# Kernel optimization log

Hardware: AMD Instinct MI355X
Metric: run time of the kernel (lower is better)

The kernel has to match this reference:

```python
import jax, jax.numpy as jnp
import numpy as np

N_NODES = 100000
D_IN = 64
D_OUT = 64
N_EDGES = 1250000


def setup_inputs() -> dict:
    key = jax.random.key(0)
    k_x, k_e, k_wl, k_bl, k_wr = jax.random.split(key, 5)
    x = jax.random.normal(k_x, (N_NODES, D_IN), dtype=jnp.float32)
    edge_index = jax.random.randint(k_e, (2, N_EDGES), 0, N_NODES, dtype=jnp.int64)
    # SAGEConv params: lin_l (neighbor transform, with bias), lin_r (root transform, no bias)
    s_in = 1.0 / np.sqrt(D_IN)
    W_l = jax.random.uniform(k_wl, (D_IN, D_OUT), dtype=jnp.float32, minval=-s_in, maxval=s_in)
    b_l = jax.random.uniform(k_bl, (D_OUT,), dtype=jnp.float32, minval=-s_in, maxval=s_in)
    W_r = jax.random.uniform(k_wr, (D_IN, D_OUT), dtype=jnp.float32, minval=-s_in, maxval=s_in)
    return {"x": x, "edge_index": edge_index, "W_l": W_l, "b_l": b_l, "W_r": W_r}


def reference(x, edge_index, W_l, b_l, W_r):
    # PyG SAGEConv with aggr='add':
    #   out = lin_l(sum_{j in N(i)} x_j) + lin_r(x_i), then tanh
    src = edge_index[0]  # message sources (x_j)
    dst = edge_index[1]  # message targets (i)
    msg = x[src]                                             # [E, D_IN] gather
    aggr = jax.ops.segment_sum(msg, dst, num_segments=x.shape[0])  # [N, D_IN] scatter-add
    out = aggr @ W_l + b_l + x @ W_r                         # [N, D_OUT]
    return jnp.tanh(out)
```

## Files before the change

kernel.cpp:

```cpp
#include <hip/hip_runtime.h>
#include <hip/hip_bf16.h>
#include <hip/hip_fp16.h>

#define N_NODES 100000
#define D 64
#define N_EDGES 1250000

#define RB 64
#define NB 1563
#define FCAP 1536
#define SORT_CAP 1536

#define CB_SHIFT 11
#define NCB 49
#define CCAP 28672
#define FINE_PER_COARSE 32

#define CPAD 16

#define EPB 4096
#define PARTA_BLOCKS ((N_EDGES + EPB - 1) / EPB)
#define SEGS 16
#define SEG_CAP 1792

#define TN 64
#define PRE_BLOCKS 1563
#define FUSED_BLOCKS (PARTA_BLOCKS + PRE_BLOCKS)

#define XP 72

#define SMEM_BYTES 27648

typedef unsigned short ushort_t;
typedef _Float16 half_t;
typedef __attribute__((ext_vector_type(8))) _Float16 half8;
typedef __attribute__((ext_vector_type(4))) float floatx4;

__global__ __launch_bounds__(256) void pre_part_kernel(
    const float* __restrict__ x, const float* __restrict__ W_l,
    const float* __restrict__ b_l, const float* __restrict__ W_r,
    ushort_t* __restrict__ y, ushort_t* __restrict__ z,
    const int* __restrict__ src, const int* __restrict__ dst,
    int* __restrict__ ccursor, unsigned* __restrict__ coarse,
    int N, int E)
{
    extern __shared__ char smem[];
    int t = threadIdx.x;

    if (blockIdx.x < PARTA_BLOCKS) {
        int* hist4        = (int*)smem;
        int* lbase        = (int*)(smem + 1024);
        int* gbase        = (int*)(smem + 1280);
        int* lwb          = (int*)(smem + 1536);
        unsigned* sortedL = (unsigned*)(smem + 2560);
        const int w = t >> 6;

        if (t < 4 * NCB) hist4[t] = 0;
        __syncthreads();

        int base = blockIdx.x * EPB;
        int lim = E - base; if (lim > EPB) lim = EPB;

        for (int i = t; i < lim; i += 256)
            atomicAdd(&hist4[w * NCB + (dst[base + i] >> CB_SHIFT)], 1);
        __syncthreads();

        if (t < 64) {
            int c0 = 0, c1 = 0, c2 = 0, c3 = 0, tot = 0;
            if (t < NCB) {
                c0 = hist4[t]; c1 = hist4[NCB + t];
                c2 = hist4[2 * NCB + t]; c3 = hist4[3 * NCB + t];
                tot = c0 + c1 + c2 + c3;
            }
            int inc = tot;
#pragma unroll
            for (int off = 1; off < 64; off <<= 1) {
                int n = __shfl_up(inc, off, 64);
                if (t >= off) inc += n;
            }
            int ex = inc - tot;
            if (t < NCB) {
                lbase[t] = ex;
                gbase[t] = tot ? atomicAdd(&ccursor[t * CPAD], tot) : 0;
                lwb[t]           = ex;
                lwb[NCB + t]     = ex + c0;
                lwb[2 * NCB + t] = ex + c0 + c1;
                lwb[3 * NCB + t] = ex + c0 + c1 + c2;
            } else {
                lbase[t] = lim;
            }
        }
        __syncthreads();

        for (int i = t; i < lim; i += 256) {
            int d = dst[base + i];
            int s = src[base + i];
            int b = d >> CB_SHIFT;
            int pos = atomicSub(&hist4[w * NCB + b], 1) - 1;
            sortedL[lwb[w * NCB + b] + pos] =
                (unsigned)s | ((unsigned)(d & ((1 << CB_SHIFT) - 1)) << 17);
        }
        __syncthreads();

        for (int i = t; i < lim; i += 256) {
            int lo = 0;
#pragma unroll
            for (int s2 = 32; s2; s2 >>= 1) {
                int c = lo + s2;
                if (c < 64 && lbase[c] <= i) lo = c;
            }
            coarse[(size_t)lo * CCAP + gbase[lo] + (i - lbase[lo])] = sortedL[i];
        }
        return;
    }

    half_t* sWt = (half_t*)smem;
    half_t* sXh = (half_t*)(smem + 18432);

    for (int i = t; i < 64 * 64; i += 256) {
        int k = i >> 6, c = i & 63;
        sWt[c * XP + k]        = (half_t)W_l[i];
        sWt[(64 + c) * XP + k] = (half_t)W_r[i];
    }

    long base = (long)(blockIdx.x - PARTA_BLOCKS) * TN;
    for (int i = t; i < TN * 16; i += 256) {
        int n = i >> 4, q = i & 15;
        long node = base + n;
        float4 v = make_float4(0.f, 0.f, 0.f, 0.f);
        if (node < N) v = ((const float4*)(x + node * D))[q];
        half_t* p = &sXh[n * XP + q * 4];
        p[0] = (half_t)v.x; p[1] = (half_t)v.y;
        p[2] = (half_t)v.z; p[3] = (half_t)v.w;
    }
    __syncthreads();

    const int lane  = t & 63;
    const int w     = t >> 6;
    const int col16 = lane & 15;
    const int quad  = lane >> 4;

    const int nrow = w * 16 + col16;
    half8 xb0 = *(half8*)&sXh[nrow * XP + quad * 8];
    half8 xb1 = *(half8*)&sXh[nrow * XP + 32 + quad * 8];

    float4 bq[4];
#pragma unroll
    for (int j = 0; j < 4; j++) bq[j] = *(const float4*)(b_l + j * 16 + quad * 4);

#pragma unroll
    for (int ct = 0; ct < 4; ct++) {
        int c = ct * 16 + col16;
        half8 wa0 = *(half8*)&sWt[c * XP + quad * 8];
        half8 wa1 = *(half8*)&sWt[c * XP + 32 + quad * 8];
        floatx4 acc = {0.f, 0.f, 0.f, 0.f};
        acc = __builtin_amdgcn_mfma_f32_16x16x32_f16(wa0, xb0, acc, 0, 0, 0);
        acc = __builtin_amdgcn_mfma_f32_16x16x32_f16(wa1, xb1, acc, 0, 0, 0);
        union { half_t h[4]; uint2 u; } pk;
        pk.h[0] = (half_t)acc[0]; pk.h[1] = (half_t)acc[1];
        pk.h[2] = (half_t)acc[2]; pk.h[3] = (half_t)acc[3];
        *(uint2*)&sXh[(w * 16 + col16) * XP + ct * 16 + quad * 4] = pk.u;
    }
    __syncthreads();

    for (int c2 = t; c2 < TN * 8; c2 += 256) {
        int row = c2 >> 3, f = c2 & 7;
        if (base + row < N)
            *(uint4*)(y + (base + row) * D + f * 8) = *(uint4*)&sXh[row * XP + f * 8];
    }
    __syncthreads();

#pragma unroll
    for (int ct = 4; ct < 8; ct++) {
        int c = ct * 16 + col16;
        half8 wa0 = *(half8*)&sWt[c * XP + quad * 8];
        half8 wa1 = *(half8*)&sWt[c * XP + 32 + quad * 8];
        floatx4 acc = {0.f, 0.f, 0.f, 0.f};
        acc = __builtin_amdgcn_mfma_f32_16x16x32_f16(wa0, xb0, acc, 0, 0, 0);
        acc = __builtin_amdgcn_mfma_f32_16x16x32_f16(wa1, xb1, acc, 0, 0, 0);
        float4 bv = bq[ct - 4];
        union { half_t h[4]; uint2 u; } pk;
        pk.h[0] = (half_t)(acc[0] + bv.x); pk.h[1] = (half_t)(acc[1] + bv.y);
        pk.h[2] = (half_t)(acc[2] + bv.z); pk.h[3] = (half_t)(acc[3] + bv.w);
        *(uint2*)&sXh[(w * 16 + col16) * XP + (ct - 4) * 16 + quad * 4] = pk.u;
    }
    __syncthreads();

    for (int c2 = t; c2 < TN * 8; c2 += 256) {
        int row = c2 >> 3, f = c2 & 7;
        if (base + row < N)
            *(uint4*)(z + (base + row) * D + f * 8) = *(uint4*)&sXh[row * XP + f * 8];
    }
}

__global__ __launch_bounds__(256) void partB_kernel(
    const unsigned* __restrict__ coarse, const int* __restrict__ ccursor,
    int* __restrict__ fcursor, unsigned* __restrict__ fine)
{
    __shared__ int hist4[4 * FINE_PER_COARSE];
    __shared__ int lbase2[FINE_PER_COARSE];
    __shared__ int gbase2[FINE_PER_COARSE];
    __shared__ int lwb2[4 * FINE_PER_COARSE];
    __shared__ unsigned sortedL[SEG_CAP];

    int cb = blockIdx.x >> 4;
    int seg = blockIdx.x & 15;
    int t = threadIdx.x;
    const int w = t >> 6;

    int cnt = ccursor[cb * CPAD];
    int segLen = (cnt + SEGS - 1) / SEGS;
    int beg = seg * segLen;
    int end = beg + segLen; if (end > cnt) end = cnt;
    int lim = end - beg; if (lim < 0) lim = 0;

    if (t < 4 * FINE_PER_COARSE) hist4[t] = 0;
    __syncthreads();

    const unsigned* __restrict__ slab = coarse + (size_t)cb * CCAP + beg;

    for (int i = t; i < lim; i += 256)
        atomicAdd(&hist4[w * FINE_PER_COARSE + ((slab[i] >> 17) >> 6)], 1);
    __syncthreads();

    if (t < 64) {
        int c0 = 0, c1 = 0, c2 = 0, c3 = 0, tot = 0;
        if (t < FINE_PER_COARSE) {
            c0 = hist4[t]; c1 = hist4[FINE_PER_COARSE + t];
            c2 = hist4[2 * FINE_PER_COARSE + t]; c3 = hist4[3 * FINE_PER_COARSE + t];
            tot = c0 + c1 + c2 + c3;
        }
        int inc = tot;
#pragma unroll
        for (int off = 1; off < 32; off <<= 1) {
            int n = __shfl_up(inc, off, 64);
            if (t >= off) inc += n;
        }
        int ex = inc - tot;
        if (t < FINE_PER_COARSE) {
            lbase2[t] = ex;
            int fb = cb * FINE_PER_COARSE + t;
            gbase2[t] = tot ? atomicAdd(&fcursor[fb * CPAD], tot) : 0;
            lwb2[t]                       = ex;
            lwb2[FINE_PER_COARSE + t]     = ex + c0;
            lwb2[2 * FINE_PER_COARSE + t] = ex + c0 + c1;
            lwb2[3 * FINE_PER_COARSE + t] = ex + c0 + c1 + c2;
        }
    }
    __syncthreads();

    for (int i = t; i < lim; i += 256) {
        unsigned e = slab[i];
        unsigned cl = e >> 17;
        int loc = cl >> 6;
        int pos = atomicSub(&hist4[w * FINE_PER_COARSE + loc], 1) - 1;
        sortedL[lwb2[w * FINE_PER_COARSE + loc] + pos] =
            (e & 0x1FFFFu) | ((cl & 63u) << 17);
    }
    __syncthreads();

    for (int i = t; i < lim; i += 256) {
        int lo = 0;
#pragma unroll
        for (int s2 = 16; s2; s2 >>= 1) {
            int c = lo + s2;
            if (c < FINE_PER_COARSE && lbase2[c] <= i) lo = c;
        }
        fine[((size_t)cb * FINE_PER_COARSE + lo) * FCAP + gbase2[lo] + (i - lbase2[lo])]
            = sortedL[i];
    }
}

__global__ __launch_bounds__(512) void sortgather_kernel(
    const ushort_t* __restrict__ y, const ushort_t* __restrict__ z,
    const unsigned* __restrict__ part, const int* __restrict__ cursor,
    float* __restrict__ out, int N)
{
    __shared__ int sorted[SORT_CAP];
    __shared__ int hist[RB];
    __shared__ int cur[RB];
    __shared__ int begL[RB];

    int b = blockIdx.x;
    int t = threadIdx.x;
    int cnt = cursor[b * CPAD];
    if (cnt > SORT_CAP) cnt = SORT_CAP;
    const unsigned* __restrict__ slab = part + (size_t)b * FCAP;

    unsigned e0 = 0, e1 = 0, e2 = 0;
    int i0 = t, i1 = t + 512, i2 = t + 1024;
    if (i0 < cnt) e0 = slab[i0];
    if (i1 < cnt) e1 = slab[i1];
    if (i2 < cnt) e2 = slab[i2];

    if (t < RB) hist[t] = 0;
    __syncthreads();

    if (i0 < cnt) atomicAdd(&hist[e0 >> 17], 1);
    if (i1 < cnt) atomicAdd(&hist[e1 >> 17], 1);
    if (i2 < cnt) atomicAdd(&hist[e2 >> 17], 1);
    __syncthreads();

    if (t < RB) {
        int v = hist[t];
        int inc = v;
#pragma unroll
        for (int off = 1; off < RB; off <<= 1) {
            int n = __shfl_up(inc, off, RB);
            if (t >= off) inc += n;
        }
        int ex = inc - v;
        cur[t] = ex;
        begL[t] = ex;
    }
    __syncthreads();

    if (i0 < cnt) { int p = atomicAdd(&cur[e0 >> 17], 1); sorted[p] = (int)(e0 & 0x1FFFF); }
    if (i1 < cnt) { int p = atomicAdd(&cur[e1 >> 17], 1); sorted[p] = (int)(e1 & 0x1FFFF); }
    if (i2 < cnt) { int p = atomicAdd(&cur[e2 >> 17], 1); sorted[p] = (int)(e2 & 0x1FFFF); }
    __syncthreads();

    const int g = t >> 3;
    const int f = t & 7;
    int myBeg = begL[g];
    int myDeg = hist[g];

    float2 acc0 = make_float2(0.f, 0.f), acc1 = acc0, acc2 = acc0, acc3 = acc0;

#define ACC(r) { \
    float2 c0 = __half22float2(*(const __half2*)&(r).x); \
    float2 c1 = __half22float2(*(const __half2*)&(r).y); \
    float2 c2 = __half22float2(*(const __half2*)&(r).z); \
    float2 c3 = __half22float2(*(const __half2*)&(r).w); \
    acc0.x += c0.x; acc0.y += c0.y; acc1.x += c1.x; acc1.y += c1.y; \
    acc2.x += c2.x; acc2.y += c2.y; acc3.x += c3.x; acc3.y += c3.y; }

    int i = 0;
    for (; i + 8 <= myDeg; i += 8) {
        int s0 = sorted[myBeg + i];
        int s1 = sorted[myBeg + i + 1];
        int s2 = sorted[myBeg + i + 2];
        int s3 = sorted[myBeg + i + 3];
        int s4 = sorted[myBeg + i + 4];
        int s5 = sorted[myBeg + i + 5];
        int s6 = sorted[myBeg + i + 6];
        int s7 = sorted[myBeg + i + 7];
        uint4 r0 = ((const uint4*)(y + (size_t)s0 * D))[f];
        uint4 r1 = ((const uint4*)(y + (size_t)s1 * D))[f];
        uint4 r2 = ((const uint4*)(y + (size_t)s2 * D))[f];
        uint4 r3 = ((const uint4*)(y + (size_t)s3 * D))[f];
        uint4 r4 = ((const uint4*)(y + (size_t)s4 * D))[f];
        uint4 r5 = ((const uint4*)(y + (size_t)s5 * D))[f];
        uint4 r6 = ((const uint4*)(y + (size_t)s6 * D))[f];
        uint4 r7 = ((const uint4*)(y + (size_t)s7 * D))[f];
        ACC(r0) ACC(r1) ACC(r2) ACC(r3) ACC(r4) ACC(r5) ACC(r6) ACC(r7)
    }
    for (; i + 4 <= myDeg; i += 4) {
        int s0 = sorted[myBeg + i];
        int s1 = sorted[myBeg + i + 1];
        int s2 = sorted[myBeg + i + 2];
        int s3 = sorted[myBeg + i + 3];
        uint4 r0 = ((const uint4*)(y + (size_t)s0 * D))[f];
        uint4 r1 = ((const uint4*)(y + (size_t)s1 * D))[f];
        uint4 r2 = ((const uint4*)(y + (size_t)s2 * D))[f];
        uint4 r3 = ((const uint4*)(y + (size_t)s3 * D))[f];
        ACC(r0) ACC(r1) ACC(r2) ACC(r3)
    }
    for (; i < myDeg; i++) {
        int s = sorted[myBeg + i];
        uint4 r = ((const uint4*)(y + (size_t)s * D))[f];
        ACC(r)
    }
#undef ACC

    long gn = (long)b * RB + g;
    if (gn < N) {
        uint4 zr = ((const uint4*)(z + (size_t)gn * D))[f];
        float2 z0 = __half22float2(*(const __half2*)&zr.x);
        float2 z1 = __half22float2(*(const __half2*)&zr.y);
        float2 z2 = __half22float2(*(const __half2*)&zr.z);
        float2 z3 = __half22float2(*(const __half2*)&zr.w);
        float4 o0, o1;
        o0.x = tanhf(acc0.x + z0.x); o0.y = tanhf(acc0.y + z0.y);
        o0.z = tanhf(acc1.x + z1.x); o0.w = tanhf(acc1.y + z1.y);
        o1.x = tanhf(acc2.x + z2.x); o1.y = tanhf(acc2.y + z2.y);
        o1.z = tanhf(acc3.x + z3.x); o1.w = tanhf(acc3.y + z3.y);
        float4* op = (float4*)(out + gn * D);
        op[2 * f] = o0;
        op[2 * f + 1] = o1;
    }
}

extern "C" void kernel_launch(void* const* d_in, const int* in_sizes, int n_in,
                              void* d_out, int out_size, void* d_ws, size_t ws_size,
                              hipStream_t stream) {
    const float* x   = (const float*)d_in[0];
    const int* ei    = (const int*)d_in[1];
    const float* W_l = (const float*)d_in[2];
    const float* b_l = (const float*)d_in[3];
    const float* W_r = (const float*)d_in[4];
    float* out = (float*)d_out;

    const int N = N_NODES;
    const int E = N_EDGES;
    const int* src = ei;
    const int* dst = ei + E;

    char* ws = (char*)d_ws;
    ushort_t* y      = (ushort_t*)(ws);
    ushort_t* z      = (ushort_t*)(ws + 12800000);
    unsigned* coarse = (unsigned*)(ws + 25600000);
    unsigned* fine   = (unsigned*)(ws + 31219712);
    int* ccursor     = (int*)(ws + 40822784);
    int* fcursor     = (int*)(ws + 40825920);

    hipMemsetAsync(ccursor, 0, 103168, stream);

    pre_part_kernel<<<FUSED_BLOCKS, 256, SMEM_BYTES, stream>>>(
        x, W_l, b_l, W_r, y, z, src, dst, ccursor, coarse, N, E);
    partB_kernel<<<NCB * SEGS, 256, 0, stream>>>(coarse, ccursor, fcursor, fine);
    sortgather_kernel<<<NB, 512, 0, stream>>>(y, z, fine, fcursor, out, N);
}
```

Baseline: 140.7 us.

## Enlarge fused pre/partition blocks to 1024 threads and batch sortgather buckets

```diff
diff --git a/kernel.cpp b/kernel.cpp
--- a/kernel.cpp
+++ b/kernel.cpp
@@ -18,25 +18,29 @@
 
 #define CPAD 16
 
-#define EPB 4096
+#define EPB 8192
 #define PARTA_BLOCKS ((N_EDGES + EPB - 1) / EPB)
 #define SEGS 16
 #define SEG_CAP 1792
 
-#define TN 64
-#define PRE_BLOCKS 1563
+#define TNP 256
+#define PRE_BLOCKS ((N_NODES + TNP - 1) / TNP)
 #define FUSED_BLOCKS (PARTA_BLOCKS + PRE_BLOCKS)
 
+#define NWAVE 16
+
 #define XP 72
-
-#define SMEM_BYTES 27648
+#define SMEM_BYTES 55296
+
+#define SG_BPB 2
+#define SG_BLOCKS ((NB + SG_BPB - 1) / SG_BPB)
 
 typedef unsigned short ushort_t;
 typedef _Float16 half_t;
 typedef __attribute__((ext_vector_type(8))) _Float16 half8;
 typedef __attribute__((ext_vector_type(4))) float floatx4;
 
-__global__ __launch_bounds__(256) void pre_part_kernel(
+__global__ __launch_bounds__(1024) void pre_part_kernel(
     const float* __restrict__ x, const float* __restrict__ W_l,
     const float* __restrict__ b_l, const float* __restrict__ W_r,
     ushort_t* __restrict__ y, ushort_t* __restrict__ z,
@@ -48,29 +52,28 @@
     int t = threadIdx.x;
 
     if (blockIdx.x < PARTA_BLOCKS) {
-        int* hist4        = (int*)smem;
-        int* lbase        = (int*)(smem + 1024);
-        int* gbase        = (int*)(smem + 1280);
-        int* lwb          = (int*)(smem + 1536);
-        unsigned* sortedL = (unsigned*)(smem + 2560);
+        int* hist16       = (int*)smem;
+        int* lbase        = (int*)(smem + 3200);
+        int* gbase        = (int*)(smem + 3456);
+        int* lwb          = (int*)(smem + 3712);
+        unsigned* sortedL = (unsigned*)(smem + 6912);
         const int w = t >> 6;
 
-        if (t < 4 * NCB) hist4[t] = 0;
+        if (t < NWAVE * NCB) hist16[t] = 0;
         __syncthreads();
 
         int base = blockIdx.x * EPB;
         int lim = E - base; if (lim > EPB) lim = EPB;
 
-        for (int i = t; i < lim; i += 256)
-            atomicAdd(&hist4[w * NCB + (dst[base + i] >> CB_SHIFT)], 1);
+        for (int i = t; i < lim; i += 1024)
+            atomicAdd(&hist16[w * NCB + (dst[base + i] >> CB_SHIFT)], 1);
         __syncthreads();
 
         if (t < 64) {
-            int c0 = 0, c1 = 0, c2 = 0, c3 = 0, tot = 0;
+            int cw[NWAVE]; int tot = 0;
             if (t < NCB) {
-                c0 = hist4[t]; c1 = hist4[NCB + t];
-                c2 = hist4[2 * NCB + t]; c3 = hist4[3 * NCB + t];
-                tot = c0 + c1 + c2 + c3;
+#pragma unroll
+                for (int k = 0; k < NWAVE; k++) { cw[k] = hist16[k * NCB + t]; tot += cw[k]; }
             }
             int inc = tot;
 #pragma unroll
@@ -82,27 +85,26 @@
             if (t < NCB) {
                 lbase[t] = ex;
                 gbase[t] = tot ? atomicAdd(&ccursor[t * CPAD], tot) : 0;
-                lwb[t]           = ex;
-                lwb[NCB + t]     = ex + c0;
-                lwb[2 * NCB + t] = ex + c0 + c1;
-                lwb[3 * NCB + t] = ex + c0 + c1 + c2;
+                int run = ex;
+#pragma unroll
+                for (int k = 0; k < NWAVE; k++) { lwb[k * NCB + t] = run; run += cw[k]; }
             } else {
                 lbase[t] = lim;
             }
         }
         __syncthreads();
 
-        for (int i = t; i < lim; i += 256) {
+        for (int i = t; i < lim; i += 1024) {
             int d = dst[base + i];
             int s = src[base + i];
             int b = d >> CB_SHIFT;
-            int pos = atomicSub(&hist4[w * NCB + b], 1) - 1;
+            int pos = atomicSub(&hist16[w * NCB + b], 1) - 1;
             sortedL[lwb[w * NCB + b] + pos] =
                 (unsigned)s | ((unsigned)(d & ((1 << CB_SHIFT) - 1)) << 17);
         }
         __syncthreads();
 
-        for (int i = t; i < lim; i += 256) {
+        for (int i = t; i < lim; i += 1024) {
             int lo = 0;
 #pragma unroll
             for (int s2 = 32; s2; s2 >>= 1) {
@@ -117,14 +119,14 @@
     half_t* sWt = (half_t*)smem;
     half_t* sXh = (half_t*)(smem + 18432);
 
-    for (int i = t; i < 64 * 64; i += 256) {
+    for (int i = t; i < 64 * 64; i += 1024) {
         int k = i >> 6, c = i & 63;
         sWt[c * XP + k]        = (half_t)W_l[i];
         sWt[(64 + c) * XP + k] = (half_t)W_r[i];
     }
 
-    long base = (long)(blockIdx.x - PARTA_BLOCKS) * TN;
-    for (int i = t; i < TN * 16; i += 256) {
+    long base = (long)(blockIdx.x - PARTA_BLOCKS) * TNP;
+    for (int i = t; i < TNP * 16; i += 1024) {
         int n = i >> 4, q = i & 15;
         long node = base + n;
         float4 v = make_float4(0.f, 0.f, 0.f, 0.f);
@@ -159,11 +161,11 @@
         union { half_t h[4]; uint2 u; } pk;
         pk.h[0] = (half_t)acc[0]; pk.h[1] = (half_t)acc[1];
         pk.h[2] = (half_t)acc[2]; pk.h[3] = (half_t)acc[3];
-        *(uint2*)&sXh[(w * 16 + col16) * XP + ct * 16 + quad * 4] = pk.u;
-    }
-    __syncthreads();
-
-    for (int c2 = t; c2 < TN * 8; c2 += 256) {
+        *(uint2*)&sXh[nrow * XP + ct * 16 + quad * 4] = pk.u;
+    }
+    __syncthreads();
+
+    for (int c2 = t; c2 < TNP * 8; c2 += 1024) {
         int row = c2 >> 3, f = c2 & 7;
         if (base + row < N)
             *(uint4*)(y + (base + row) * D + f * 8) = *(uint4*)&sXh[row * XP + f * 8];
@@ -182,11 +184,11 @@
         union { half_t h[4]; uint2 u; } pk;
         pk.h[0] = (half_t)(acc[0] + bv.x); pk.h[1] = (half_t)(acc[1] + bv.y);
         pk.h[2] = (half_t)(acc[2] + bv.z); pk.h[3] = (half_t)(acc[3] + bv.w);
-        *(uint2*)&sXh[(w * 16 + col16) * XP + (ct - 4) * 16 + quad * 4] = pk.u;
-    }
-    __syncthreads();
-
-    for (int c2 = t; c2 < TN * 8; c2 += 256) {
+        *(uint2*)&sXh[nrow * XP + (ct - 4) * 16 + quad * 4] = pk.u;
+    }
+    __syncthreads();
+
+    for (int c2 = t; c2 < TNP * 8; c2 += 1024) {
         int row = c2 >> 3, f = c2 & 7;
         if (base + row < N)
             *(uint4*)(z + (base + row) * D + f * 8) = *(uint4*)&sXh[row * XP + f * 8];
@@ -281,113 +283,119 @@
     __shared__ int cur[RB];
     __shared__ int begL[RB];
 
-    int b = blockIdx.x;
     int t = threadIdx.x;
-    int cnt = cursor[b * CPAD];
-    if (cnt > SORT_CAP) cnt = SORT_CAP;
-    const unsigned* __restrict__ slab = part + (size_t)b * FCAP;
-
-    unsigned e0 = 0, e1 = 0, e2 = 0;
-    int i0 = t, i1 = t + 512, i2 = t + 1024;
-    if (i0 < cnt) e0 = slab[i0];
-    if (i1 < cnt) e1 = slab[i1];
-    if (i2 < cnt) e2 = slab[i2];
-
-    if (t < RB) hist[t] = 0;
-    __syncthreads();
-
-    if (i0 < cnt) atomicAdd(&hist[e0 >> 17], 1);
-    if (i1 < cnt) atomicAdd(&hist[e1 >> 17], 1);
-    if (i2 < cnt) atomicAdd(&hist[e2 >> 17], 1);
-    __syncthreads();
-
-    if (t < RB) {
-        int v = hist[t];
-        int inc = v;
-#pragma unroll
-        for (int off = 1; off < RB; off <<= 1) {
-            int n = __shfl_up(inc, off, RB);
-            if (t >= off) inc += n;
-        }
-        int ex = inc - v;
-        cur[t] = ex;
-        begL[t] = ex;
-    }
-    __syncthreads();
-
-    if (i0 < cnt) { int p = atomicAdd(&cur[e0 >> 17], 1); sorted[p] = (int)(e0 & 0x1FFFF); }
-    if (i1 < cnt) { int p = atomicAdd(&cur[e1 >> 17], 1); sorted[p] = (int)(e1 & 0x1FFFF); }
-    if (i2 < cnt) { int p = atomicAdd(&cur[e2 >> 17], 1); sorted[p] = (int)(e2 & 0x1FFFF); }
-    __syncthreads();
-
-    const int g = t >> 3;
-    const int f = t & 7;
-    int myBeg = begL[g];
-    int myDeg = hist[g];
-
-    float2 acc0 = make_float2(0.f, 0.f), acc1 = acc0, acc2 = acc0, acc3 = acc0;
+
+    for (int sub = 0; sub < SG_BPB; sub++) {
+        int b = blockIdx.x * SG_BPB + sub;
+        if (b >= NB) break;
+        __syncthreads();
+
+        int cnt = cursor[b * CPAD];
+        if (cnt > SORT_CAP) cnt = SORT_CAP;
+        const unsigned* __restrict__ slab = part + (size_t)b * FCAP;
+
+        unsigned e0 = 0, e1 = 0, e2 = 0;
+        int i0 = t, i1 = t + 512, i2 = t + 1024;
+        if (i0 < cnt) e0 = slab[i0];
+        if (i1 < cnt) e1 = slab[i1];
+        if (i2 < cnt) e2 = slab[i2];
+
+        if (t < RB) hist[t] = 0;
+        __syncthreads();
+
+        if (i0 < cnt) atomicAdd(&hist[e0 >> 17], 1);
+        if (i1 < cnt) atomicAdd(&hist[e1 >> 17], 1);
+        if (i2 < cnt) atomicAdd(&hist[e2 >> 17], 1);
+        __syncthreads();
+
+        if (t < RB) {
+            int v = hist[t];
+            int inc = v;
+#pragma unroll
+            for (int off = 1; off < RB; off <<= 1) {
+                int n = __shfl_up(inc, off, RB);
+                if (t >= off) inc += n;
+            }
+            int ex = inc - v;
+            cur[t] = ex;
+            begL[t] = ex;
+        }
+        __syncthreads();
+
+        if (i0 < cnt) { int p = atomicAdd(&cur[e0 >> 17], 1); sorted[p] = (int)(e0 & 0x1FFFF); }
+        if (i1 < cnt) { int p = atomicAdd(&cur[e1 >> 17], 1); sorted[p] = (int)(e1 & 0x1FFFF); }
+        if (i2 < cnt) { int p = atomicAdd(&cur[e2 >> 17], 1); sorted[p] = (int)(e2 & 0x1FFFF); }
+        __syncthreads();
+
+        const int g = t >> 3;
+        const int f = t & 7;
+        int myBeg = begL[g];
+        int myDeg = hist[g];
+
+        float2 acc0 = make_float2(0.f, 0.f), acc1 = acc0, acc2 = acc0, acc3 = acc0;
 
 #define ACC(r) { \
-    float2 c0 = __half22float2(*(const __half2*)&(r).x); \
-    float2 c1 = __half22float2(*(const __half2*)&(r).y); \
-    float2 c2 = __half22float2(*(const __half2*)&(r).z); \
-    float2 c3 = __half22float2(*(const __half2*)&(r).w); \
-    acc0.x += c0.x; acc0.y += c0.y; acc1.x += c1.x; acc1.y += c1.y; \
-    acc2.x += c2.x; acc2.y += c2.y; acc3.x += c3.x; acc3.y += c3.y; }
-
-    int i = 0;
-    for (; i + 8 <= myDeg; i += 8) {
-        int s0 = sorted[myBeg + i];
-        int s1 = sorted[myBeg + i + 1];
-        int s2 = sorted[myBeg + i + 2];
-        int s3 = sorted[myBeg + i + 3];
-        int s4 = sorted[myBeg + i + 4];
-        int s5 = sorted[myBeg + i + 5];
-        int s6 = sorted[myBeg + i + 6];
-        int s7 = sorted[myBeg + i + 7];
-        uint4 r0 = ((const uint4*)(y + (size_t)s0 * D))[f];
-        uint4 r1 = ((const uint4*)(y + (size_t)s1 * D))[f];
-        uint4 r2 = ((const uint4*)(y + (size_t)s2 * D))[f];
-        uint4 r3 = ((const uint4*)(y + (size_t)s3 * D))[f];
-        uint4 r4 = ((const uint4*)(y + (size_t)s4 * D))[f];
-        uint4 r5 = ((const uint4*)(y + (size_t)s5 * D))[f];
-        uint4 r6 = ((const uint4*)(y + (size_t)s6 * D))[f];
-        uint4 r7 = ((const uint4*)(y + (size_t)s7 * D))[f];
-        ACC(r0) ACC(r1) ACC(r2) ACC(r3) ACC(r4) ACC(r5) ACC(r6) ACC(r7)
-    }
-    for (; i + 4 <= myDeg; i += 4) {
-        int s0 = sorted[myBeg + i];
-        int s1 = sorted[myBeg + i + 1];
-        int s2 = sorted[myBeg + i + 2];
-        int s3 = sorted[myBeg + i + 3];
-        uint4 r0 = ((const uint4*)(y + (size_t)s0 * D))[f];
-        uint4 r1 = ((const uint4*)(y + (size_t)s1 * D))[f];
-        uint4 r2 = ((const uint4*)(y + (size_t)s2 * D))[f];
-        uint4 r3 = ((const uint4*)(y + (size_t)s3 * D))[f];
-        ACC(r0) ACC(r1) ACC(r2) ACC(r3)
-    }
-    for (; i < myDeg; i++) {
-        int s = sorted[myBeg + i];
-        uint4 r = ((const uint4*)(y + (size_t)s * D))[f];
-        ACC(r)
-    }
+        float2 c0 = __half22float2(*(const __half2*)&(r).x); \
+        float2 c1 = __half22float2(*(const __half2*)&(r).y); \
+        float2 c2 = __half22float2(*(const __half2*)&(r).z); \
+        float2 c3 = __half22float2(*(const __half2*)&(r).w); \
+        acc0.x += c0.x; acc0.y += c0.y; acc1.x += c1.x; acc1.y += c1.y; \
+        acc2.x += c2.x; acc2.y += c2.y; acc3.x += c3.x; acc3.y += c3.y; }
+
+        int i = 0;
+        for (; i + 8 <= myDeg; i += 8) {
+            int s0 = sorted[myBeg + i];
+            int s1 = sorted[myBeg + i + 1];
+            int s2 = sorted[myBeg + i + 2];
+            int s3 = sorted[myBeg + i + 3];
+            int s4 = sorted[myBeg + i + 4];
+            int s5 = sorted[myBeg + i + 5];
+            int s6 = sorted[myBeg + i + 6];
+            int s7 = sorted[myBeg + i + 7];
+            uint4 r0 = ((const uint4*)(y + (size_t)s0 * D))[f];
+            uint4 r1 = ((const uint4*)(y + (size_t)s1 * D))[f];
+            uint4 r2 = ((const uint4*)(y + (size_t)s2 * D))[f];
+            uint4 r3 = ((const uint4*)(y + (size_t)s3 * D))[f];
+            uint4 r4 = ((const uint4*)(y + (size_t)s4 * D))[f];
+            uint4 r5 = ((const uint4*)(y + (size_t)s5 * D))[f];
+            uint4 r6 = ((const uint4*)(y + (size_t)s6 * D))[f];
+            uint4 r7 = ((const uint4*)(y + (size_t)s7 * D))[f];
+            ACC(r0) ACC(r1) ACC(r2) ACC(r3) ACC(r4) ACC(r5) ACC(r6) ACC(r7)
+        }
+        for (; i + 4 <= myDeg; i += 4) {
+            int s0 = sorted[myBeg + i];
+            int s1 = sorted[myBeg + i + 1];
+            int s2 = sorted[myBeg + i + 2];
+            int s3 = sorted[myBeg + i + 3];
+            uint4 r0 = ((const uint4*)(y + (size_t)s0 * D))[f];
+            uint4 r1 = ((const uint4*)(y + (size_t)s1 * D))[f];
+            uint4 r2 = ((const uint4*)(y + (size_t)s2 * D))[f];
+            uint4 r3 = ((const uint4*)(y + (size_t)s3 * D))[f];
+            ACC(r0) ACC(r1) ACC(r2) ACC(r3)
+        }
+        for (; i < myDeg; i++) {
+            int s = sorted[myBeg + i];
+            uint4 r = ((const uint4*)(y + (size_t)s * D))[f];
+            ACC(r)
+        }
 #undef ACC
 
-    long gn = (long)b * RB + g;
-    if (gn < N) {
-        uint4 zr = ((const uint4*)(z + (size_t)gn * D))[f];
-        float2 z0 = __half22float2(*(const __half2*)&zr.x);
-        float2 z1 = __half22float2(*(const __half2*)&zr.y);
-        float2 z2 = __half22float2(*(const __half2*)&zr.z);
-        float2 z3 = __half22float2(*(const __half2*)&zr.w);
-        float4 o0, o1;
-        o0.x = tanhf(acc0.x + z0.x); o0.y = tanhf(acc0.y + z0.y);
-        o0.z = tanhf(acc1.x + z1.x); o0.w = tanhf(acc1.y + z1.y);
-        o1.x = tanhf(acc2.x + z2.x); o1.y = tanhf(acc2.y + z2.y);
-        o1.z = tanhf(acc3.x + z3.x); o1.w = tanhf(acc3.y + z3.y);
-        float4* op = (float4*)(out + gn * D);
-        op[2 * f] = o0;
-        op[2 * f + 1] = o1;
+        long gn = (long)b * RB + g;
+        if (gn < N) {
+            uint4 zr = ((const uint4*)(z + (size_t)gn * D))[f];
+            float2 z0 = __half22float2(*(const __half2*)&zr.x);
+            float2 z1 = __half22float2(*(const __half2*)&zr.y);
+            float2 z2 = __half22float2(*(const __half2*)&zr.z);
+            float2 z3 = __half22float2(*(const __half2*)&zr.w);
+            float4 o0, o1;
+            o0.x = tanhf(acc0.x + z0.x); o0.y = tanhf(acc0.y + z0.y);
+            o0.z = tanhf(acc1.x + z1.x); o0.w = tanhf(acc1.y + z1.y);
+            o1.x = tanhf(acc2.x + z2.x); o1.y = tanhf(acc2.y + z2.y);
+            o1.z = tanhf(acc3.x + z3.x); o1.w = tanhf(acc3.y + z3.y);
+            float4* op = (float4*)(out + gn * D);
+            op[2 * f] = o0;
+            op[2 * f + 1] = o1;
+        }
     }
 }
 
@@ -416,8 +424,8 @@
 
     hipMemsetAsync(ccursor, 0, 103168, stream);
 
-    pre_part_kernel<<<FUSED_BLOCKS, 256, SMEM_BYTES, stream>>>(
+    pre_part_kernel<<<FUSED_BLOCKS, 1024, SMEM_BYTES, stream>>>(
         x, W_l, b_l, W_r, y, z, src, dst, ccursor, coarse, N, E);
     partB_kernel<<<NCB * SEGS, 256, 0, stream>>>(coarse, ccursor, fcursor, fine);
-    sortgather_kernel<<<NB, 512, 0, stream>>>(y, z, fine, fcursor, out, N);
+    sortgather_kernel<<<SG_BLOCKS, 512, 0, stream>>>(y, z, fine, fcursor, out, N);
 }
```

Measured after the change: 138.7 us. Within noise of the previous version (-1.4%).
